# Kernel optimization log

Hardware: AMD Instinct MI355X
Metric: run time of the kernel (lower is better)

Reference implementation:

```python
import jax, jax.numpy as jnp
import numpy as np

N_HEADS = 16
ROPE_DIMS = 16
SEQ_LEN = 512


def _rope_cache(T, dtype=jnp.float32):
    rd = ROPE_DIMS
    freqs = 1.0 / (10000.0 ** (jnp.arange(0, rd, 2, dtype=jnp.float32) / rd))  # [rd/2]
    t = jnp.arange(T, dtype=jnp.float32)
    ang = jnp.outer(t, freqs)  # [T, rd/2]
    return jnp.cos(ang).astype(dtype), jnp.sin(ang).astype(dtype)


def _apply_rope(x, cos, sin):
    # x: [B, H, T, hd]; partial RoPE on first ROPE_DIMS dims
    rd = ROPE_DIMS
    x_rope, x_pass = x[..., :rd], x[..., rd:]
    x1, x2 = x_rope[..., : rd // 2], x_rope[..., rd // 2 :]
    # cos/sin: [T, rd/2] -> broadcast over B, H
    out = jnp.concatenate([x1 * cos - x2 * sin, x2 * cos + x1 * sin], axis=-1)
    return jnp.concatenate([out, x_pass], axis=-1)


def setup_inputs() -> dict:
    key = jax.random.key(0)
    k1, k2, k3 = jax.random.split(key, 3)
    B, T, C = 8, SEQ_LEN, 2048
    x = jax.random.normal(k1, (B, T, C), dtype=jnp.float32)
    Wqkv = jax.random.normal(k2, (3 * C, C), dtype=jnp.float32) * (1.0 / np.sqrt(C))
    Wout = jax.random.normal(k3, (C, C), dtype=jnp.float32) * (1.0 / np.sqrt(C))
    return {"x": x, "Wqkv": Wqkv, "Wout": Wout}


def reference(x, Wqkv, Wout):
    B, T, C = x.shape
    H = N_HEADS
    hd = C // H
    # fused QKV projection
    qkv = jnp.einsum("btc,fc->btf", x, Wqkv)  # [B, T, 3C]
    qkv = qkv.reshape(B, T, 3, H, hd)
    q, k, v = qkv[:, :, 0], qkv[:, :, 1], qkv[:, :, 2]  # [B, T, H, hd]
    q = jnp.transpose(q, (0, 2, 1, 3))  # [B, H, T, hd]
    k = jnp.transpose(k, (0, 2, 1, 3))
    v = jnp.transpose(v, (0, 2, 1, 3))
    cos, sin = _rope_cache(T, dtype=x.dtype)
    q = _apply_rope(q, cos, sin)
    k = _apply_rope(k, cos, sin)
    # causal SDPA
    scale = 1.0 / np.sqrt(hd)
    scores = jnp.einsum("bhqd,bhkd->bhqk", q, k) * scale
    causal = jnp.tril(jnp.ones((T, T), dtype=bool))
    scores = jnp.where(causal, scores, jnp.finfo(scores.dtype).min)
    attn = jax.nn.softmax(scores, axis=-1)
    y = jnp.einsum("bhqk,bhkd->bhqd", attn, v)  # [B, H, T, hd]
    y = jnp.transpose(y, (0, 2, 1, 3)).reshape(B, T, C)
    return jnp.einsum("btc,oc->bto", y, Wout)
```

## Files before the change

### kernel.cpp

```cpp
#include <hip/hip_runtime.h>

typedef __bf16 bf16_t;
typedef __bf16 bf16x4 __attribute__((ext_vector_type(4)));
typedef __bf16 bf16x8 __attribute__((ext_vector_type(8)));
typedef float f32x4 __attribute__((ext_vector_type(4)));

#define GLB(p) ((const __attribute__((address_space(1))) void*)(p))
#define LDS(p) ((__attribute__((address_space(3))) void*)(p))

__global__ void f32_to_bf16(const float* __restrict__ src, bf16_t* __restrict__ dst, int n8)
{
    const int i = blockIdx.x * 256 + threadIdx.x;
    if (i >= n8) return;
    const f32x4 a = *(const f32x4*)&src[(size_t)i * 8];
    const f32x4 b = *(const f32x4*)&src[(size_t)i * 8 + 4];
    bf16x8 h = {(bf16_t)a[0], (bf16_t)a[1], (bf16_t)a[2], (bf16_t)a[3],
                (bf16_t)b[0], (bf16_t)b[1], (bf16_t)b[2], (bf16_t)b[3]};
    *(bf16x8*)&dst[(size_t)i * 8] = h;
}

#define LDB4(d, kk, S)                                                         \
    { _Pragma("unroll") for (int nt = 0; nt < 4; ++nt)                         \
        bfr[S][nt] = *(const bf16x8*)&smem[sBe + (d) * 32768 + (kk) * 8192 + nt * 512]; }

#define LDA4(d, kk, g, S)                                                      \
    { _Pragma("unroll") for (int i = 0; i < 4; ++i)                            \
        afr[S][i] = *(const bf16x8*)&smem[sAe + (d) * 32768 + (kk) * 8192 + ((g) * 4 + i) * 512]; }

#define MM4(g, SA, SB)                                                         \
    { _Pragma("unroll") for (int i = 0; i < 4; ++i)                            \
        _Pragma("unroll") for (int nt = 0; nt < 4; ++nt)                       \
            acc[(g) * 4 + i][nt] = __builtin_amdgcn_mfma_f32_16x16x32_bf16(    \
                afr[SA][i], bfr[SB][nt], acc[(g) * 4 + i][nt], 0, 0, 0); }

#define PHASE_TAIL(g, SA, SB)                                                  \
    __builtin_amdgcn_s_barrier();                                              \
    asm volatile("s_waitcnt lgkmcnt(0)" ::: "memory");                         \
    __builtin_amdgcn_s_setprio(1);                                             \
    MM4(g, SA, SB);                                                            \
    __builtin_amdgcn_s_setprio(0);                                             \
    __builtin_amdgcn_s_barrier();

template <int MODE>
__global__ __launch_bounds__(512, 2)
void gemm256(const bf16_t* __restrict__ A, const bf16_t* __restrict__ Bm, int K,
             bf16_t* __restrict__ o0, bf16_t* __restrict__ o1, bf16_t* __restrict__ o2,
             float* __restrict__ of)
{
    __shared__ __align__(16) bf16_t smem[65536];

    const int tid  = threadIdx.x;
    const int lane = tid & 63;
    const int w    = tid >> 6;
    const int wr   = w >> 2;
    const int wc   = w & 3;
    const int quad = lane >> 4;
    const int qcol = lane & 15;
    const int m0   = blockIdx.x * 256;
    const int n0   = blockIdx.y * 256;

    f32x4 acc[8][4];
#pragma unroll
    for (int i = 0; i < 8; ++i)
#pragma unroll
        for (int j = 0; j < 4; ++j)
            acc[i][j] = (f32x4){0.f, 0.f, 0.f, 0.f};

    const int srow = w * 16 + (lane >> 2);
    const int scg  = (lane & 3) ^ ((lane >> 3) & 3);
    const bf16_t* Ag = A  + (size_t)(m0 + srow) * K + scg * 8;
    const bf16_t* Bg = Bm + (size_t)(n0 + srow) * K + scg * 8;

    auto STAGE = [&](int d, int t, int hh) {
        const int isA = hh & 1;
        const int kh  = hh >> 1;
        const bf16_t* g = (isA ? Ag : Bg) + t * 64 + kh * 32;
        bf16_t* l = &smem[d * 32768 + kh * 8192 + (isA ? 0 : 16384) + w * 512];
        __builtin_amdgcn_global_load_lds(GLB(g), LDS(l), 16, 0, 0);
        __builtin_amdgcn_global_load_lds(GLB(g + (size_t)128 * K), LDS(l + 4096), 16, 0, 0);
    };

    const int rs8 = (quad ^ ((qcol >> 1) & 3)) * 8;
    const int sAe = (wr * 128 + qcol) * 32 + rs8;
    const int sBe = 16384 + (wc * 64 + qcol) * 32 + rs8;

    bf16x8 afr[2][4], bfr[2][4];

    const int NT  = K >> 6;
    const int NIT = NT >> 1;

    STAGE(0, 0, 0); STAGE(0, 0, 1); STAGE(0, 0, 2); STAGE(0, 0, 3);
    STAGE(1, 1, 0); STAGE(1, 1, 1); STAGE(1, 1, 2);
    asm volatile("s_waitcnt vmcnt(6)" ::: "memory");
    __builtin_amdgcn_s_barrier();

    for (int J = 0; J < NIT - 1; ++J) {
        const int t = 2 * J;
        LDB4(0, 0, 0); LDA4(0, 0, 0, 0); STAGE(1, t + 1, 3);
        PHASE_TAIL(0, 0, 0);
        LDA4(0, 0, 1, 1); STAGE(0, t + 2, 0);
        PHASE_TAIL(1, 1, 0);
        LDB4(0, 1, 1); LDA4(0, 1, 0, 0); STAGE(0, t + 2, 1);
        PHASE_TAIL(0, 0, 1);
        LDA4(0, 1, 1, 1); STAGE(0, t + 2, 2);
        asm volatile("s_waitcnt vmcnt(6)" ::: "memory");
        PHASE_TAIL(1, 1, 1);
        LDB4(1, 0, 0); LDA4(1, 0, 0, 0); STAGE(0, t + 2, 3);
        PHASE_TAIL(0, 0, 0);
        LDA4(1, 0, 1, 1); STAGE(1, t + 3, 0);
        PHASE_TAIL(1, 1, 0);
        LDB4(1, 1, 1); LDA4(1, 1, 0, 0); STAGE(1, t + 3, 1);
        PHASE_TAIL(0, 0, 1);
        LDA4(1, 1, 1, 1); STAGE(1, t + 3, 2);
        asm volatile("s_waitcnt vmcnt(6)" ::: "memory");
        PHASE_TAIL(1, 1, 1);
    }

    {
        const int t = NT - 2;
        LDB4(0, 0, 0); LDA4(0, 0, 0, 0); STAGE(1, t + 1, 3);
        PHASE_TAIL(0, 0, 0);
        LDA4(0, 0, 1, 1);
        PHASE_TAIL(1, 1, 0);
        LDB4(0, 1, 1); LDA4(0, 1, 0, 0);
        PHASE_TAIL(0, 0, 1);
        LDA4(0, 1, 1, 1);
        asm volatile("s_waitcnt vmcnt(0)" ::: "memory");
        PHASE_TAIL(1, 1, 1);
        LDB4(1, 0, 0); LDA4(1, 0, 0, 0);
        PHASE_TAIL(0, 0, 0);
        LDA4(1, 0, 1, 1);
        PHASE_TAIL(1, 1, 0);
        LDB4(1, 1, 1); LDA4(1, 1, 0, 0);
        PHASE_TAIL(0, 0, 1);
        LDA4(1, 1, 1, 1);
        __builtin_amdgcn_s_barrier();
        asm volatile("s_waitcnt lgkmcnt(0)" ::: "memory");
        __builtin_amdgcn_s_setprio(1);
        MM4(1, 1, 1);
        __builtin_amdgcn_s_setprio(0);
    }

#pragma unroll
    for (int mt = 0; mt < 8; ++mt) {
#pragma unroll
        for (int nt = 0; nt < 4; ++nt) {
#pragma unroll
            for (int r = 0; r < 4; ++r) {
                const int m = m0 + wr * 128 + mt * 16 + quad * 4 + r;
                const int f = n0 + wc * 64 + nt * 16 + qcol;
                const float val = acc[mt][nt][r];
                if (MODE == 0) {
                    const int b     = m >> 9;
                    const int t     = m & 511;
                    const int which = f >> 11;
                    const int h     = (f >> 7) & 15;
                    const int d     = f & 127;
                    if (which == 2) {
                        o2[((size_t)(((b << 4) + h) * 128 + d) << 9) + t] = (bf16_t)val;
                    } else {
                        bf16_t* dst = (which == 0) ? o0 : o1;
                        dst[(size_t)(((b << 4) + h) * 512 + t) * 128 + d] = (bf16_t)val;
                    }
                } else {
                    of[(size_t)m * 2048 + f] = val;
                }
            }
        }
    }
}

template <int MODE>
__global__ __launch_bounds__(256)
void gemm_bt(const bf16_t* __restrict__ A, const bf16_t* __restrict__ Bm, int K,
             bf16_t* __restrict__ o0, bf16_t* __restrict__ o1, bf16_t* __restrict__ o2,
             float* __restrict__ of)
{
    __shared__ __align__(16) bf16_t As[128 * 32];
    __shared__ __align__(16) bf16_t Bs[128 * 32];
    const int tid  = threadIdx.x;
    const int lane = tid & 63;
    const int w    = tid >> 6;
    const int wm   = (w & 1) * 64;
    const int wn   = (w >> 1) * 64;
    const int m0   = blockIdx.x * 128;
    const int n0   = blockIdx.y * 128;
    const int quad = lane >> 4;
    const int qcol = lane & 15;

    f32x4 acc[4][4];
#pragma unroll
    for (int i = 0; i < 4; ++i)
#pragma unroll
        for (int j = 0; j < 4; ++j)
            acc[i][j] = (f32x4){0.f, 0.f, 0.f, 0.f};

    const int rc = lane >> 2;
    const int cg = (lane & 3) ^ (rc & 3);
    const int c0 = 2 * w, c1 = 2 * w + 1;
    const bf16_t* ag0 = A  + (size_t)(m0 + 16 * c0 + rc) * K + cg * 8;
    const bf16_t* ag1 = A  + (size_t)(m0 + 16 * c1 + rc) * K + cg * 8;
    const bf16_t* bg0 = Bm + (size_t)(n0 + 16 * c0 + rc) * K + cg * 8;
    const bf16_t* bg1 = Bm + (size_t)(n0 + 16 * c1 + rc) * K + cg * 8;
    bf16_t* al0 = &As[c0 * 512];
    bf16_t* al1 = &As[c1 * 512];
    bf16_t* bl0 = &Bs[c0 * 512];
    bf16_t* bl1 = &Bs[c1 * 512];

    const int swz8 = (quad ^ (qcol & 3)) * 8;

    for (int k0 = 0; k0 < K; k0 += 32) {
        __syncthreads();
        __builtin_amdgcn_global_load_lds(GLB(ag0 + k0), LDS(al0), 16, 0, 0);
        __builtin_amdgcn_global_load_lds(GLB(ag1 + k0), LDS(al1), 16, 0, 0);
        __builtin_amdgcn_global_load_lds(GLB(bg0 + k0), LDS(bl0), 16, 0, 0);
        __builtin_amdgcn_global_load_lds(GLB(bg1 + k0), LDS(bl1), 16, 0, 0);
        __syncthreads();

        bf16x8 af[4], bf[4];
#pragma unroll
        for (int mt = 0; mt < 4; ++mt)
            af[mt] = *(const bf16x8*)&As[(wm + mt * 16 + qcol) * 32 + swz8];
#pragma unroll
        for (int nt = 0; nt < 4; ++nt)
            bf[nt] = *(const bf16x8*)&Bs[(wn + nt * 16 + qcol) * 32 + swz8];
#pragma unroll
        for (int mt = 0; mt < 4; ++mt)
#pragma unroll
            for (int nt = 0; nt < 4; ++nt)
                acc[mt][nt] = __builtin_amdgcn_mfma_f32_16x16x32_bf16(af[mt], bf[nt], acc[mt][nt], 0, 0, 0);
    }

#pragma unroll
    for (int mt = 0; mt < 4; ++mt) {
#pragma unroll
        for (int nt = 0; nt < 4; ++nt) {
#pragma unroll
            for (int r = 0; r < 4; ++r) {
                const int m = m0 + wm + mt * 16 + quad * 4 + r;
                const int f = n0 + wn + nt * 16 + qcol;
                const float val = acc[mt][nt][r];
                of[(size_t)m * 2048 + f] = val;
            }
        }
    }
}

__global__ void rope_kernel(bf16_t* __restrict__ q, bf16_t* __restrict__ k)
{
    const int id  = blockIdx.x * 256 + threadIdx.x;
    const int arr = id >> 19;
    const int rem = id & ((1 << 19) - 1);
    const int bh  = rem >> 12;
    const int t   = (rem >> 3) & 511;
    const int d   = rem & 7;

    bf16_t* p = (arr ? k : q) + (size_t)(bh * 512 + t) * 128;
    const float x1 = (float)p[d];
    const float x2 = (float)p[d + 8];
    const float freq = __expf(-(float)d * 1.1512925464970229f);
    const float ang  = (float)t * freq;
    const float c = cosf(ang), s = sinf(ang);
    p[d]     = (bf16_t)(x1 * c - x2 * s);
    p[d + 8] = (bf16_t)(x2 * c + x1 * s);
}

#define KLD 136
#define VLD 72
#define PLD 72

__global__ __launch_bounds__(512)
void flash_attn(const bf16_t* __restrict__ q, const bf16_t* __restrict__ k,
                const bf16_t* __restrict__ vT, bf16_t* __restrict__ y)
{
    const int qtb = blockIdx.x;
    const int h   = blockIdx.y;
    const int b   = blockIdx.z;
    const int tid  = threadIdx.x;
    const int lane = tid & 63;
    const int w    = tid >> 6;
    const int quad = lane >> 4;
    const int qcol = lane & 15;

    __shared__ __align__(16) bf16_t Ks[64 * KLD];
    __shared__ __align__(16) bf16_t VTs[128 * VLD];
    __shared__ __align__(16) bf16_t Ps[256 * PLD];
    __shared__ __align__(16) float aS[8][2][16];
    __shared__ __align__(16) float lS[8][2][16];

    const bf16_t* qb  = q  + (size_t)((b * 16 + h) * 512) * 128;
    const bf16_t* kb  = k  + (size_t)((b * 16 + h) * 512) * 128;
    const bf16_t* vtb = vT + (size_t)((b * 16 + h) * 128) * 512;

    bf16x8 qfrag[2][4];
#pragma unroll
    for (int qg = 0; qg < 2; ++qg) {
        const int qrow = qtb * 256 + w * 32 + qg * 16 + qcol;
#pragma unroll
        for (int kc = 0; kc < 4; ++kc)
            qfrag[qg][kc] = *(const bf16x8*)&qb[(size_t)qrow * 128 + kc * 32 + quad * 8];
    }

    f32x4 acc_o[2][8];
#pragma unroll
    for (int qg = 0; qg < 2; ++qg)
#pragma unroll
        for (int nt = 0; nt < 8; ++nt) acc_o[qg][nt] = (f32x4){0.f, 0.f, 0.f, 0.f};
    float m_run[2] = {-INFINITY, -INFINITY};
    float l_run[2] = {0.f, 0.f};
    const float scale = 0.08838834764831845f;

    const int wq_min  = qtb * 256 + w * 32;
    const int kt_last = 4 * qtb + 3;
    for (int kt = 0; kt <= kt_last; ++kt) {
        __syncthreads();
#pragma unroll
        for (int p = 0; p < 2; ++p) {
            const int r = p * 32 + (tid >> 4), c = (tid & 15) * 8;
            *(uint4*)&Ks[r * KLD + c] = *(const uint4*)&kb[(size_t)(kt * 64 + r) * 128 + c];
        }
#pragma unroll
        for (int p = 0; p < 2; ++p) {
            const int r = p * 64 + (tid >> 3), c = (tid & 7) * 8;
            *(uint4*)&VTs[r * VLD + c] = *(const uint4*)&vtb[(size_t)r * 512 + kt * 64 + c];
        }
        __syncthreads();

        if (kt * 64 > wq_min + 31) continue;
        const bool need_mask = ((kt + 1) * 64 > wq_min);

#pragma unroll
        for (int qg = 0; qg < 2; ++qg) {
            f32x4 sacc[4];
#pragma unroll
            for (int mt = 0; mt < 4; ++mt) sacc[mt] = (f32x4){0.f, 0.f, 0.f, 0.f};
#pragma unroll
            for (int mt = 0; mt < 4; ++mt)
#pragma unroll
                for (int kc = 0; kc < 4; ++kc) {
                    bf16x8 af = *(const bf16x8*)&Ks[(mt * 16 + qcol) * KLD + kc * 32 + quad * 8];
                    sacc[mt] = __builtin_amdgcn_mfma_f32_16x16x32_bf16(af, qfrag[qg][kc], sacc[mt], 0, 0, 0);
                }

            float s[16];
#pragma unroll
            for (int mt = 0; mt < 4; ++mt)
#pragma unroll
                for (int r = 0; r < 4; ++r)
                    s[mt * 4 + r] = sacc[mt][r] * scale;
            if (need_mask) {
                const int qglob = qtb * 256 + w * 32 + qg * 16 + qcol;
#pragma unroll
                for (int mt = 0; mt < 4; ++mt)
#pragma unroll
                    for (int r = 0; r < 4; ++r)
                        if (kt * 64 + mt * 16 + quad * 4 + r > qglob)
                            s[mt * 4 + r] = -1e30f;
            }

            float mx = s[0];
#pragma unroll
            for (int i = 1; i < 16; ++i) mx = fmaxf(mx, s[i]);
            mx = fmaxf(mx, __shfl_xor(mx, 16));
            mx = fmaxf(mx, __shfl_xor(mx, 32));
            const float m_new = fmaxf(m_run[qg], mx);
            const float alpha = __expf(m_run[qg] - m_new);
            float p16[16];
            float sum = 0.f;
#pragma unroll
            for (int i = 0; i < 16; ++i) { p16[i] = __expf(s[i] - m_new); sum += p16[i]; }
            sum += __shfl_xor(sum, 16);
            sum += __shfl_xor(sum, 32);
            l_run[qg] = l_run[qg] * alpha + sum;
            m_run[qg] = m_new;
            if (quad == 0) aS[w][qg][qcol] = alpha;

#pragma unroll
            for (int mt = 0; mt < 4; ++mt) {
                bf16x4 pb = {(bf16_t)p16[mt * 4 + 0], (bf16_t)p16[mt * 4 + 1],
                             (bf16_t)p16[mt * 4 + 2], (bf16_t)p16[mt * 4 + 3]};
                *(bf16x4*)&Ps[(w * 32 + qg * 16 + qcol) * PLD + mt * 16 + quad * 4] = pb;
            }

            f32x4 alpha4 = *(const f32x4*)&aS[w][qg][quad * 4];
#pragma unroll
            for (int nt = 0; nt < 8; ++nt)
#pragma unroll
                for (int r = 0; r < 4; ++r)
                    acc_o[qg][nt][r] *= alpha4[r];

#pragma unroll
            for (int kc2 = 0; kc2 < 2; ++kc2) {
                bf16x8 pf = *(const bf16x8*)&Ps[(w * 32 + qg * 16 + qcol) * PLD + kc2 * 32 + quad * 8];
#pragma unroll
                for (int nt = 0; nt < 8; ++nt) {
                    bf16x8 vf = *(const bf16x8*)&VTs[(nt * 16 + qcol) * VLD + kc2 * 32 + quad * 8];
                    acc_o[qg][nt] = __builtin_amdgcn_mfma_f32_16x16x32_bf16(pf, vf, acc_o[qg][nt], 0, 0, 0);
                }
            }
        }
    }

    if (quad == 0) { lS[w][0][qcol] = l_run[0]; lS[w][1][qcol] = l_run[1]; }
#pragma unroll
    for (int qg = 0; qg < 2; ++qg) {
        f32x4 l4 = *(const f32x4*)&lS[w][qg][quad * 4];
#pragma unroll
        for (int nt = 0; nt < 8; ++nt)
#pragma unroll
            for (int r = 0; r < 4; ++r) {
                const int t  = qtb * 256 + w * 32 + qg * 16 + quad * 4 + r;
                const int cc = h * 128 + nt * 16 + qcol;
                y[(size_t)(b * 512 + t) * 2048 + cc] = (bf16_t)(acc_o[qg][nt][r] / l4[r]);
            }
    }
}

extern "C" void kernel_launch(void* const* d_in, const int* in_sizes, int n_in,
                              void* d_out, int out_size, void* d_ws, size_t ws_size,
                              hipStream_t stream)
{
    (void)in_sizes; (void)n_in; (void)out_size; (void)ws_size;

    const float* x    = (const float*)d_in[0];
    const float* Wqkv = (const float*)d_in[1];
    const float* Wout = (const float*)d_in[2];
    float* out = (float*)d_out;

    const size_t SEG = (size_t)8 * 16 * 512 * 128;
    bf16_t* q      = (bf16_t*)d_ws;
    bf16_t* k      = q + SEG;
    bf16_t* vT     = k + SEG;
    bf16_t* xb     = vT + SEG;
    bf16_t* y      = xb;
    bf16_t* Wqkvb  = xb + SEG;
    bf16_t* Woutb  = Wqkvb + (size_t)6144 * 2048;

    f32_to_bf16<<<(8388608 / 8) / 256, 256, 0, stream>>>(x, xb, 8388608 / 8);
    f32_to_bf16<<<(12582912 / 8) / 256, 256, 0, stream>>>(Wqkv, Wqkvb, 12582912 / 8);
    f32_to_bf16<<<(4194304 / 8) / 256, 256, 0, stream>>>(Wout, Woutb, 4194304 / 8);
    gemm256<0><<<dim3(4096 / 256, 6144 / 256), 512, 0, stream>>>(xb, Wqkvb, 2048, q, k, vT, nullptr);
    rope_kernel<<<(2 * 128 * 512 * 8) / 256, 256, 0, stream>>>(q, k);
    flash_attn<<<dim3(2, 16, 8), 512, 0, stream>>>(q, k, vT, y);
    gemm_bt<1><<<dim3(4096 / 128, 2048 / 128), 256, 0, stream>>>(y, Woutb, 2048, nullptr, nullptr, nullptr, out);
}
```

Baseline: 360.6 us.

## Restructure flash attention into smaller blocks reading K/V directly from global

Flash attention now launches 512 blocks of 256 threads, each covering 128 query rows instead of 256, and orders block IDs so heavy and light causal tiles interleave. K and V^T fragments are loaded straight from global memory into MFMA operands, which removes the LDS staging and the two barriers per key tile. Both query groups share each K/V fragment load. Softmax alpha and the final row sum are broadcast with shuffles instead of LDS. The aim is better occupancy and load balance with no block-wide syncs, at the cost of redundant global and L2 reads of K/V across waves.

```diff
diff --git a/kernel.cpp b/kernel.cpp
--- a/kernel.cpp
+++ b/kernel.cpp
@@ -265,28 +265,25 @@
     p[d + 8] = (bf16_t)(x2 * c + x1 * s);
 }
 
-#define KLD 136
-#define VLD 72
 #define PLD 72
 
-__global__ __launch_bounds__(512)
+__global__ __launch_bounds__(256)
 void flash_attn(const bf16_t* __restrict__ q, const bf16_t* __restrict__ k,
                 const bf16_t* __restrict__ vT, bf16_t* __restrict__ y)
 {
-    const int qtb = blockIdx.x;
-    const int h   = blockIdx.y;
-    const int b   = blockIdx.z;
+    const int bid = blockIdx.x;
+    const int sg  = bid >> 7;
+    const int qtb = (sg < 2) ? sg : 5 - sg;
+    const int rem = bid & 127;
+    const int h   = rem & 15;
+    const int b   = rem >> 4;
     const int tid  = threadIdx.x;
     const int lane = tid & 63;
     const int w    = tid >> 6;
     const int quad = lane >> 4;
     const int qcol = lane & 15;
 
-    __shared__ __align__(16) bf16_t Ks[64 * KLD];
-    __shared__ __align__(16) bf16_t VTs[128 * VLD];
-    __shared__ __align__(16) bf16_t Ps[256 * PLD];
-    __shared__ __align__(16) float aS[8][2][16];
-    __shared__ __align__(16) float lS[8][2][16];
+    __shared__ __align__(16) bf16_t Ps[128 * PLD];
 
     const bf16_t* qb  = q  + (size_t)((b * 16 + h) * 512) * 128;
     const bf16_t* kb  = k  + (size_t)((b * 16 + h) * 512) * 128;
@@ -295,7 +292,7 @@
     bf16x8 qfrag[2][4];
 #pragma unroll
     for (int qg = 0; qg < 2; ++qg) {
-        const int qrow = qtb * 256 + w * 32 + qg * 16 + qcol;
+        const int qrow = qtb * 128 + w * 32 + qg * 16 + qcol;
 #pragma unroll
         for (int kc = 0; kc < 4; ++kc)
             qfrag[qg][kc] = *(const bf16x8*)&qb[(size_t)qrow * 128 + kc * 32 + quad * 8];
@@ -310,46 +307,36 @@
     float l_run[2] = {0.f, 0.f};
     const float scale = 0.08838834764831845f;
 
-    const int wq_min  = qtb * 256 + w * 32;
-    const int kt_last = 4 * qtb + 3;
+    const int wq_min  = qtb * 128 + w * 32;
+    const int kt_last = 2 * qtb + 1;
     for (int kt = 0; kt <= kt_last; ++kt) {
-        __syncthreads();
-#pragma unroll
-        for (int p = 0; p < 2; ++p) {
-            const int r = p * 32 + (tid >> 4), c = (tid & 15) * 8;
-            *(uint4*)&Ks[r * KLD + c] = *(const uint4*)&kb[(size_t)(kt * 64 + r) * 128 + c];
-        }
-#pragma unroll
-        for (int p = 0; p < 2; ++p) {
-            const int r = p * 64 + (tid >> 3), c = (tid & 7) * 8;
-            *(uint4*)&VTs[r * VLD + c] = *(const uint4*)&vtb[(size_t)r * 512 + kt * 64 + c];
-        }
-        __syncthreads();
-
-        if (kt * 64 > wq_min + 31) continue;
+        if (kt * 64 > wq_min + 31) break;
         const bool need_mask = ((kt + 1) * 64 > wq_min);
 
+        f32x4 sacc[2][4];
+#pragma unroll
+        for (int qg = 0; qg < 2; ++qg)
+#pragma unroll
+            for (int mt = 0; mt < 4; ++mt) sacc[qg][mt] = (f32x4){0.f, 0.f, 0.f, 0.f};
+#pragma unroll
+        for (int mt = 0; mt < 4; ++mt)
+#pragma unroll
+            for (int kc = 0; kc < 4; ++kc) {
+                bf16x8 af = *(const bf16x8*)&kb[(size_t)(kt * 64 + mt * 16 + qcol) * 128 + kc * 32 + quad * 8];
+                sacc[0][mt] = __builtin_amdgcn_mfma_f32_16x16x32_bf16(af, qfrag[0][kc], sacc[0][mt], 0, 0, 0);
+                sacc[1][mt] = __builtin_amdgcn_mfma_f32_16x16x32_bf16(af, qfrag[1][kc], sacc[1][mt], 0, 0, 0);
+            }
+
 #pragma unroll
         for (int qg = 0; qg < 2; ++qg) {
-            f32x4 sacc[4];
-#pragma unroll
-            for (int mt = 0; mt < 4; ++mt) sacc[mt] = (f32x4){0.f, 0.f, 0.f, 0.f};
+            float s[16];
 #pragma unroll
             for (int mt = 0; mt < 4; ++mt)
 #pragma unroll
-                for (int kc = 0; kc < 4; ++kc) {
-                    bf16x8 af = *(const bf16x8*)&Ks[(mt * 16 + qcol) * KLD + kc * 32 + quad * 8];
-                    sacc[mt] = __builtin_amdgcn_mfma_f32_16x16x32_bf16(af, qfrag[qg][kc], sacc[mt], 0, 0, 0);
-                }
-
-            float s[16];
-#pragma unroll
-            for (int mt = 0; mt < 4; ++mt)
-#pragma unroll
                 for (int r = 0; r < 4; ++r)
-                    s[mt * 4 + r] = sacc[mt][r] * scale;
+                    s[mt * 4 + r] = sacc[qg][mt][r] * scale;
             if (need_mask) {
-                const int qglob = qtb * 256 + w * 32 + qg * 16 + qcol;
+                const int qglob = qtb * 128 + w * 32 + qg * 16 + qcol;
 #pragma unroll
                 for (int mt = 0; mt < 4; ++mt)
 #pragma unroll
@@ -373,7 +360,6 @@
             sum += __shfl_xor(sum, 32);
             l_run[qg] = l_run[qg] * alpha + sum;
             m_run[qg] = m_new;
-            if (quad == 0) aS[w][qg][qcol] = alpha;
 
 #pragma unroll
             for (int mt = 0; mt < 4; ++mt) {
@@ -382,37 +368,40 @@
                 *(bf16x4*)&Ps[(w * 32 + qg * 16 + qcol) * PLD + mt * 16 + quad * 4] = pb;
             }
 
-            f32x4 alpha4 = *(const f32x4*)&aS[w][qg][quad * 4];
-#pragma unroll
-            for (int nt = 0; nt < 8; ++nt)
-#pragma unroll
-                for (int r = 0; r < 4; ++r)
-                    acc_o[qg][nt][r] *= alpha4[r];
-
-#pragma unroll
-            for (int kc2 = 0; kc2 < 2; ++kc2) {
-                bf16x8 pf = *(const bf16x8*)&Ps[(w * 32 + qg * 16 + qcol) * PLD + kc2 * 32 + quad * 8];
-#pragma unroll
-                for (int nt = 0; nt < 8; ++nt) {
-                    bf16x8 vf = *(const bf16x8*)&VTs[(nt * 16 + qcol) * VLD + kc2 * 32 + quad * 8];
-                    acc_o[qg][nt] = __builtin_amdgcn_mfma_f32_16x16x32_bf16(pf, vf, acc_o[qg][nt], 0, 0, 0);
-                }
+#pragma unroll
+            for (int r = 0; r < 4; ++r) {
+                const float ar = __shfl(alpha, quad * 4 + r);
+#pragma unroll
+                for (int nt = 0; nt < 8; ++nt)
+                    acc_o[qg][nt][r] *= ar;
             }
         }
-    }
-
-    if (quad == 0) { lS[w][0][qcol] = l_run[0]; lS[w][1][qcol] = l_run[1]; }
+
+#pragma unroll
+        for (int kc2 = 0; kc2 < 2; ++kc2) {
+            bf16x8 pf0 = *(const bf16x8*)&Ps[(w * 32 + qcol) * PLD + kc2 * 32 + quad * 8];
+            bf16x8 pf1 = *(const bf16x8*)&Ps[(w * 32 + 16 + qcol) * PLD + kc2 * 32 + quad * 8];
+#pragma unroll
+            for (int nt = 0; nt < 8; ++nt) {
+                bf16x8 vf = *(const bf16x8*)&vtb[(size_t)(nt * 16 + qcol) * 512 + kt * 64 + kc2 * 32 + quad * 8];
+                acc_o[0][nt] = __builtin_amdgcn_mfma_f32_16x16x32_bf16(pf0, vf, acc_o[0][nt], 0, 0, 0);
+                acc_o[1][nt] = __builtin_amdgcn_mfma_f32_16x16x32_bf16(pf1, vf, acc_o[1][nt], 0, 0, 0);
+            }
+        }
+    }
+
 #pragma unroll
     for (int qg = 0; qg < 2; ++qg) {
-        f32x4 l4 = *(const f32x4*)&lS[w][qg][quad * 4];
-#pragma unroll
-        for (int nt = 0; nt < 8; ++nt)
-#pragma unroll
-            for (int r = 0; r < 4; ++r) {
-                const int t  = qtb * 256 + w * 32 + qg * 16 + quad * 4 + r;
+#pragma unroll
+        for (int r = 0; r < 4; ++r) {
+            const float lr = __shfl(l_run[qg], quad * 4 + r);
+            const int t  = qtb * 128 + w * 32 + qg * 16 + quad * 4 + r;
+#pragma unroll
+            for (int nt = 0; nt < 8; ++nt) {
                 const int cc = h * 128 + nt * 16 + qcol;
-                y[(size_t)(b * 512 + t) * 2048 + cc] = (bf16_t)(acc_o[qg][nt][r] / l4[r]);
-            }
+                y[(size_t)(b * 512 + t) * 2048 + cc] = (bf16_t)(acc_o[qg][nt][r] / lr);
+            }
+        }
     }
 }
 
@@ -441,6 +430,6 @@
     f32_to_bf16<<<(4194304 / 8) / 256, 256, 0, stream>>>(Wout, Woutb, 4194304 / 8);
     gemm256<0><<<dim3(4096 / 256, 6144 / 256), 512, 0, stream>>>(xb, Wqkvb, 2048, q, k, vT, nullptr);
     rope_kernel<<<(2 * 128 * 512 * 8) / 256, 256, 0, stream>>>(q, k);
-    flash_attn<<<dim3(2, 16, 8), 512, 0, stream>>>(q, k, vT, y);
+    flash_attn<<<512, 256, 0, stream>>>(q, k, vT, y);
     gemm_bt<1><<<dim3(4096 / 128, 2048 / 128), 256, 0, stream>>>(y, Woutb, 2048, nullptr, nullptr, nullptr, out);
 }
```

After: 381.3 us. +5.7%, slower.

## Prefetch K/V tiles into registers and batch PV MFMAs in flash attention

Applied to the files above, without the earlier changes.

The K and V^T tiles for the next iteration are loaded into registers right after the barrier, so global memory latency overlaps with compute instead of stalling before each LDS store. The alpha and l broadcasts now go through __shfl, which removes the aS/lS shared arrays. The PV MFMAs for both query groups are interleaved after the softmax loop so each V fragment is reused twice. MFMA sections are wrapped in s_setprio. In exchange, register pressure rises from the prefetch buffers, which may reduce occupancy.

```diff
diff --git a/kernel.cpp b/kernel.cpp
--- a/kernel.cpp
+++ b/kernel.cpp
@@ -285,8 +285,6 @@
     __shared__ __align__(16) bf16_t Ks[64 * KLD];
     __shared__ __align__(16) bf16_t VTs[128 * VLD];
     __shared__ __align__(16) bf16_t Ps[256 * PLD];
-    __shared__ __align__(16) float aS[8][2][16];
-    __shared__ __align__(16) float lS[8][2][16];
 
     const bf16_t* qb  = q  + (size_t)((b * 16 + h) * 512) * 128;
     const bf16_t* kb  = k  + (size_t)((b * 16 + h) * 512) * 128;
@@ -310,21 +308,34 @@
     float l_run[2] = {0.f, 0.f};
     const float scale = 0.08838834764831845f;
 
+    const int krow = tid >> 4;
+    const int kcol = (tid & 15) * 8;
+    const int vrow = tid >> 3;
+    const int vcol = (tid & 7) * 8;
+    uint4 kreg[2], vreg[2];
+    auto ISSUE = [&](int kt) {
+#pragma unroll
+        for (int p = 0; p < 2; ++p)
+            kreg[p] = *(const uint4*)&kb[(size_t)(kt * 64 + p * 32 + krow) * 128 + kcol];
+#pragma unroll
+        for (int p = 0; p < 2; ++p)
+            vreg[p] = *(const uint4*)&vtb[(size_t)(p * 64 + vrow) * 512 + kt * 64 + vcol];
+    };
+
     const int wq_min  = qtb * 256 + w * 32;
     const int kt_last = 4 * qtb + 3;
+
+    ISSUE(0);
     for (int kt = 0; kt <= kt_last; ++kt) {
         __syncthreads();
 #pragma unroll
-        for (int p = 0; p < 2; ++p) {
-            const int r = p * 32 + (tid >> 4), c = (tid & 15) * 8;
-            *(uint4*)&Ks[r * KLD + c] = *(const uint4*)&kb[(size_t)(kt * 64 + r) * 128 + c];
-        }
-#pragma unroll
-        for (int p = 0; p < 2; ++p) {
-            const int r = p * 64 + (tid >> 3), c = (tid & 7) * 8;
-            *(uint4*)&VTs[r * VLD + c] = *(const uint4*)&vtb[(size_t)r * 512 + kt * 64 + c];
-        }
+        for (int p = 0; p < 2; ++p)
+            *(uint4*)&Ks[(p * 32 + krow) * KLD + kcol] = kreg[p];
+#pragma unroll
+        for (int p = 0; p < 2; ++p)
+            *(uint4*)&VTs[(p * 64 + vrow) * VLD + vcol] = vreg[p];
         __syncthreads();
+        if (kt < kt_last) ISSUE(kt + 1);
 
         if (kt * 64 > wq_min + 31) continue;
         const bool need_mask = ((kt + 1) * 64 > wq_min);
@@ -334,6 +345,7 @@
             f32x4 sacc[4];
 #pragma unroll
             for (int mt = 0; mt < 4; ++mt) sacc[mt] = (f32x4){0.f, 0.f, 0.f, 0.f};
+            __builtin_amdgcn_s_setprio(1);
 #pragma unroll
             for (int mt = 0; mt < 4; ++mt)
 #pragma unroll
@@ -341,6 +353,7 @@
                     bf16x8 af = *(const bf16x8*)&Ks[(mt * 16 + qcol) * KLD + kc * 32 + quad * 8];
                     sacc[mt] = __builtin_amdgcn_mfma_f32_16x16x32_bf16(af, qfrag[qg][kc], sacc[mt], 0, 0, 0);
                 }
+            __builtin_amdgcn_s_setprio(0);
 
             float s[16];
 #pragma unroll
@@ -373,7 +386,6 @@
             sum += __shfl_xor(sum, 32);
             l_run[qg] = l_run[qg] * alpha + sum;
             m_run[qg] = m_new;
-            if (quad == 0) aS[w][qg][qcol] = alpha;
 
 #pragma unroll
             for (int mt = 0; mt < 4; ++mt) {
@@ -382,37 +394,42 @@
                 *(bf16x4*)&Ps[(w * 32 + qg * 16 + qcol) * PLD + mt * 16 + quad * 4] = pb;
             }
 
-            f32x4 alpha4 = *(const f32x4*)&aS[w][qg][quad * 4];
-#pragma unroll
-            for (int nt = 0; nt < 8; ++nt)
-#pragma unroll
-                for (int r = 0; r < 4; ++r)
-                    acc_o[qg][nt][r] *= alpha4[r];
-
-#pragma unroll
-            for (int kc2 = 0; kc2 < 2; ++kc2) {
-                bf16x8 pf = *(const bf16x8*)&Ps[(w * 32 + qg * 16 + qcol) * PLD + kc2 * 32 + quad * 8];
-#pragma unroll
-                for (int nt = 0; nt < 8; ++nt) {
-                    bf16x8 vf = *(const bf16x8*)&VTs[(nt * 16 + qcol) * VLD + kc2 * 32 + quad * 8];
-                    acc_o[qg][nt] = __builtin_amdgcn_mfma_f32_16x16x32_bf16(pf, vf, acc_o[qg][nt], 0, 0, 0);
-                }
+#pragma unroll
+            for (int r = 0; r < 4; ++r) {
+                const float ar = __shfl(alpha, quad * 4 + r);
+#pragma unroll
+                for (int nt = 0; nt < 8; ++nt)
+                    acc_o[qg][nt][r] *= ar;
             }
         }
-    }
-
-    if (quad == 0) { lS[w][0][qcol] = l_run[0]; lS[w][1][qcol] = l_run[1]; }
+
+        __builtin_amdgcn_s_setprio(1);
+#pragma unroll
+        for (int kc2 = 0; kc2 < 2; ++kc2) {
+            bf16x8 pf0 = *(const bf16x8*)&Ps[(w * 32 + qcol) * PLD + kc2 * 32 + quad * 8];
+            bf16x8 pf1 = *(const bf16x8*)&Ps[(w * 32 + 16 + qcol) * PLD + kc2 * 32 + quad * 8];
+#pragma unroll
+            for (int nt = 0; nt < 8; ++nt) {
+                bf16x8 vf = *(const bf16x8*)&VTs[(nt * 16 + qcol) * VLD + kc2 * 32 + quad * 8];
+                acc_o[0][nt] = __builtin_amdgcn_mfma_f32_16x16x32_bf16(pf0, vf, acc_o[0][nt], 0, 0, 0);
+                acc_o[1][nt] = __builtin_amdgcn_mfma_f32_16x16x32_bf16(pf1, vf, acc_o[1][nt], 0, 0, 0);
+            }
+        }
+        __builtin_amdgcn_s_setprio(0);
+    }
+
 #pragma unroll
     for (int qg = 0; qg < 2; ++qg) {
-        f32x4 l4 = *(const f32x4*)&lS[w][qg][quad * 4];
-#pragma unroll
-        for (int nt = 0; nt < 8; ++nt)
-#pragma unroll
-            for (int r = 0; r < 4; ++r) {
-                const int t  = qtb * 256 + w * 32 + qg * 16 + quad * 4 + r;
+#pragma unroll
+        for (int r = 0; r < 4; ++r) {
+            const float lr = __shfl(l_run[qg], quad * 4 + r);
+            const int t  = qtb * 256 + w * 32 + qg * 16 + quad * 4 + r;
+#pragma unroll
+            for (int nt = 0; nt < 8; ++nt) {
                 const int cc = h * 128 + nt * 16 + qcol;
-                y[(size_t)(b * 512 + t) * 2048 + cc] = (bf16_t)(acc_o[qg][nt][r] / l4[r]);
-            }
+                y[(size_t)(b * 512 + t) * 2048 + cc] = (bf16_t)(acc_o[qg][nt][r] / lr);
+            }
+        }
     }
 }
 
```

New measurement: 378.0 us. +4.8%, slower.
